# Kernel optimization log

Measured on AMD Instinct MI355X. Metric: run time of the kernel, lower is better.

The kernel has to match this reference:

```python
import math
import jax, jax.numpy as jnp
import numpy as np

B, N_COLS, CHANNELS, NUM_HEADS = 512, 128, 512, 8
D_HEAD = CHANNELS // NUM_HEADS


def setup_inputs() -> dict:
    key = jax.random.key(0)
    ks = jax.random.split(key, 9)
    s = 1.0 / math.sqrt(CHANNELS)
    x = jax.random.normal(ks[0], (B, N_COLS, CHANNELS), dtype=jnp.float32)
    Wq = jax.random.uniform(ks[1], (CHANNELS, CHANNELS), jnp.float32, -s, s)
    bq = jax.random.uniform(ks[2], (CHANNELS,), jnp.float32, -s, s)
    Wk = jax.random.uniform(ks[3], (CHANNELS, CHANNELS), jnp.float32, -s, s)
    bk = jax.random.uniform(ks[4], (CHANNELS,), jnp.float32, -s, s)
    Wv = jax.random.uniform(ks[5], (CHANNELS, CHANNELS), jnp.float32, -s, s)
    bv = jax.random.uniform(ks[6], (CHANNELS,), jnp.float32, -s, s)
    Wo = jax.random.uniform(ks[7], (CHANNELS, CHANNELS), jnp.float32, -s, s)
    bo = jax.random.uniform(ks[8], (CHANNELS,), jnp.float32, -s, s)
    return {"x": x, "Wq": Wq, "bq": bq, "Wk": Wk, "bk": bk,
            "Wv": Wv, "bv": bv, "Wo": Wo, "bo": bo}


def reference(x, Wq, bq, Wk, bk, Wv, bv, Wo, bo):
    b, n, c = x.shape
    h, d = NUM_HEADS, D_HEAD

    def split_heads(t):  # [b, n, c] -> [b, h, n, d]
        return t.reshape(b, n, h, d).transpose(0, 2, 1, 3)

    Q = split_heads(x @ Wq + bq)
    K = split_heads(x @ Wk + bk)
    V = split_heads(x @ Wv + bv)

    # raw scores [b, h, q, k]
    scores = jnp.einsum('bhqd,bhkd->bhqk', Q, K)
    # causal mask over columns; note: mask added BEFORE scaling by sqrt(d)
    causal = jnp.tril(jnp.ones((n, n), dtype=jnp.float32))
    mask = (1.0 - causal) * -100000.0
    attn = jax.nn.softmax((scores + mask) / math.sqrt(d), axis=-1)
    out = jnp.einsum('bhqk,bhkd->bhqd', attn, V)
    out = out.transpose(0, 2, 1, 3).reshape(b, n, c)
    return out @ Wo + bo
```

## Files before the change

### kernel.cpp

```cpp
#include <hip/hip_runtime.h>

typedef _Float16 f16;
typedef _Float16 half8 __attribute__((ext_vector_type(8)));
typedef _Float16 half4 __attribute__((ext_vector_type(4)));
typedef float f32x4 __attribute__((ext_vector_type(4)));

#define B_SZ 512
#define NQ   128
#define CH   512
#define NH   8
#define DH   64
#define MTOK (B_SZ*NQ)
#define KD   512

#define MFMA16(a,b,c) __builtin_amdgcn_mfma_f32_16x16x32_f16((a),(b),(c),0,0,0)

#define GLDS16(g,l) __builtin_amdgcn_global_load_lds( \
    (__attribute__((address_space(1))) void*)(g), \
    (__attribute__((address_space(3))) void*)(l), 16, 0, 0)

__global__ __launch_bounds__(256) void k_cvt(const float* __restrict__ x,
                                             f16* __restrict__ xb) {
  const int n8 = MTOK * KD / 8;
  int i = blockIdx.x * blockDim.x + threadIdx.x;
  const int stride = gridDim.x * blockDim.x;
  for (; i < n8; i += stride) {
    f32x4 a = ((const f32x4*)x)[2 * i];
    f32x4 b = ((const f32x4*)x)[2 * i + 1];
    half8 h;
    h[0] = (f16)a[0]; h[1] = (f16)a[1]; h[2] = (f16)a[2]; h[3] = (f16)a[3];
    h[4] = (f16)b[0]; h[5] = (f16)b[1]; h[6] = (f16)b[2]; h[7] = (f16)b[3];
    ((half8*)xb)[i] = h;
  }
}

__global__ __launch_bounds__(256) void k_wt(const float* __restrict__ Wq,
                                            const float* __restrict__ Wk,
                                            const float* __restrict__ Wv,
                                            const float* __restrict__ Wo,
                                            f16* __restrict__ wt) {
  const int n = blockIdx.x;
  const float* W = (n < 512) ? Wq : (n < 1024) ? Wk : (n < 1536) ? Wv : Wo;
  const int c = n & 511;
  for (int k = threadIdx.x; k < 512; k += blockDim.x)
    wt[n * 512 + k] = (f16)W[k * 512 + c];
}

__global__ __launch_bounds__(256, 2) void k_qkv(
    f16* __restrict__ A, f16* __restrict__ Bw,
    const float* __restrict__ bq, const float* __restrict__ bk,
    const float* __restrict__ bv,
    f16* __restrict__ qb, f16* __restrict__ kb, f16* __restrict__ vb) {
  __shared__ f16 la[128 * 32];
  __shared__ f16 lb[128 * 32];
  const int tid = threadIdx.x;
  const int w = tid >> 6, lane = tid & 63;
  const int ln = lane & 15, g = lane >> 4;
  const int wr = w >> 1, wc = w & 1;
  const int mtile = blockIdx.y, ntile = blockIdx.x;

  const int e0 = w * 512 + lane * 8;
  const int srow = e0 >> 5, scol = e0 & 31;
  f16* gA = A + (mtile * 128 + srow) * KD + scol;
  f16* gB = Bw + (ntile * 128 + srow) * KD + scol;
  f16* lA = la + w * 512;
  f16* lB = lb + w * 512;

  f32x4 acc[4][4] = {};

  for (int kt = 0; kt < 16; ++kt) {
    const int k0 = kt * 32;
    GLDS16(gA + k0, lA);
    GLDS16(gA + 64 * KD + k0, lA + 2048);
    GLDS16(gB + k0, lB);
    GLDS16(gB + 64 * KD + k0, lB + 2048);
    __syncthreads();
    half8 af[4], bf[4];
#pragma unroll
    for (int m = 0; m < 4; ++m)
      af[m] = *(const half8*)(la + (wr * 64 + m * 16 + ln) * 32 + g * 8);
#pragma unroll
    for (int n = 0; n < 4; ++n)
      bf[n] = *(const half8*)(lb + (wc * 64 + n * 16 + ln) * 32 + g * 8);
#pragma unroll
    for (int m = 0; m < 4; ++m)
#pragma unroll
      for (int n = 0; n < 4; ++n)
        acc[m][n] = MFMA16(af[m], bf[n], acc[m][n]);
    __syncthreads();
  }

  const int b = mtile;
  const int colbase = ntile * 128 + wc * 64;
#pragma unroll
  for (int m = 0; m < 4; ++m) {
    const int nn0 = wr * 64 + m * 16 + g * 4;
#pragma unroll
    for (int n = 0; n < 4; ++n) {
      const int col = colbase + n * 16 + ln;
      const int which = col >> 9;
      const int c = col & 511;
      const int h = c >> 6, d = c & 63;
      const float bias = (which == 0) ? bq[c] : (which == 1) ? bk[c] : bv[c];
      if (which < 2) {
        f16* dst = ((which == 0) ? qb : kb) + ((b * NH + h) * NQ + nn0) * DH + d;
#pragma unroll
        for (int r = 0; r < 4; ++r)
          dst[r * DH] = (f16)(acc[m][n][r] + bias);
      } else {
        half4 v4;
#pragma unroll
        for (int r = 0; r < 4; ++r)
          v4[r] = (f16)(acc[m][n][r] + bias);
        *(half4*)(vb + ((b * NH + h) * DH + d) * NQ + nn0) = v4;
      }
    }
  }
}

__global__ __launch_bounds__(256, 2) void k_attn(
    const f16* __restrict__ qbuf, const f16* __restrict__ kbuf,
    const f16* __restrict__ vbuf, f16* __restrict__ ao) {
  __shared__ f16 kl[128 * 72];
  __shared__ f16 vl[64 * 136];
  __shared__ f16 pl[128 * 136];
  const int bh = blockIdx.x;
  const f16* Qp = qbuf + bh * (NQ * DH);
  const f16* Kp = kbuf + bh * (NQ * DH);
  const f16* Vp = vbuf + bh * (DH * NQ);
  const int tid = threadIdx.x;
  const int w = tid >> 6, lane = tid & 63;
  const int ln = lane & 15, g = lane >> 4;

#pragma unroll
  for (int i = 0; i < 4; ++i) {
    const int e = i * 2048 + tid * 8;
    *(half8*)(kl + (e >> 6) * 72 + (e & 63)) = *(const half8*)(Kp + e);
  }
#pragma unroll
  for (int i = 0; i < 4; ++i) {
    const int e = i * 2048 + tid * 8;
    *(half8*)(vl + (e >> 7) * 136 + (e & 127)) = *(const half8*)(Vp + e);
  }
  half8 qf[2][2];
#pragma unroll
  for (int m = 0; m < 2; ++m)
#pragma unroll
    for (int ks = 0; ks < 2; ++ks)
      qf[m][ks] = *(const half8*)(Qp + (w * 32 + m * 16 + ln) * DH + ks * 32 + g * 8);
  __syncthreads();

  f32x4 s[2][8] = {};
#pragma unroll
  for (int ks = 0; ks < 2; ++ks)
#pragma unroll
    for (int n = 0; n < 8; ++n) {
      half8 kf = *(const half8*)(kl + (n * 16 + ln) * 72 + ks * 32 + g * 8);
      s[0][n] = MFMA16(qf[0][ks], kf, s[0][n]);
      s[1][n] = MFMA16(qf[1][ks], kf, s[1][n]);
    }

  float inv[2][4];
#pragma unroll
  for (int m = 0; m < 2; ++m) {
#pragma unroll
    for (int r = 0; r < 4; ++r) {
      const int q = w * 32 + m * 16 + g * 4 + r;
      float z[8];
      float rm = -1e30f;
#pragma unroll
      for (int n = 0; n < 8; ++n) {
        const int col = n * 16 + ln;
        float zz = s[m][n][r] * 0.125f + ((col > q) ? -12500.0f : 0.0f);
        z[n] = zz;
        rm = fmaxf(rm, zz);
      }
      rm = fmaxf(rm, __shfl_xor(rm, 1));
      rm = fmaxf(rm, __shfl_xor(rm, 2));
      rm = fmaxf(rm, __shfl_xor(rm, 4));
      rm = fmaxf(rm, __shfl_xor(rm, 8));
      float rs = 0.f;
#pragma unroll
      for (int n = 0; n < 8; ++n) {
        const float p = __expf(z[n] - rm);
        rs += p;
        pl[q * 136 + n * 16 + ln] = (f16)p;
      }
      rs += __shfl_xor(rs, 1);
      rs += __shfl_xor(rs, 2);
      rs += __shfl_xor(rs, 4);
      rs += __shfl_xor(rs, 8);
      inv[m][r] = 1.0f / rs;
    }
  }

  f32x4 o[2][4] = {};
#pragma unroll
  for (int ks = 0; ks < 4; ++ks) {
    half8 pf0 = *(const half8*)(pl + (w * 32 + ln) * 136 + ks * 32 + g * 8);
    half8 pf1 = *(const half8*)(pl + (w * 32 + 16 + ln) * 136 + ks * 32 + g * 8);
#pragma unroll
    for (int n = 0; n < 4; ++n) {
      half8 vf = *(const half8*)(vl + (n * 16 + ln) * 136 + ks * 32 + g * 8);
      o[0][n] = MFMA16(pf0, vf, o[0][n]);
      o[1][n] = MFMA16(pf1, vf, o[1][n]);
    }
  }

  const int b = bh >> 3, h = bh & 7;
  f16* dst = ao + (b * NQ) * CH + h * DH;
#pragma unroll
  for (int m = 0; m < 2; ++m)
#pragma unroll
    for (int n = 0; n < 4; ++n)
#pragma unroll
      for (int r = 0; r < 4; ++r) {
        const int q = w * 32 + m * 16 + g * 4 + r;
        dst[q * CH + n * 16 + ln] = (f16)(o[m][n][r] * inv[m][r]);
      }
}

__global__ __launch_bounds__(256, 2) void k_out(
    f16* __restrict__ A, f16* __restrict__ Bw,
    const float* __restrict__ bo, float* __restrict__ out) {
  __shared__ f16 la[128 * 32];
  __shared__ f16 lb[128 * 32];
  const int tid = threadIdx.x;
  const int w = tid >> 6, lane = tid & 63;
  const int ln = lane & 15, g = lane >> 4;
  const int wr = w >> 1, wc = w & 1;
  const int mtile = blockIdx.y, ntile = blockIdx.x;

  const int e0 = w * 512 + lane * 8;
  const int srow = e0 >> 5, scol = e0 & 31;
  f16* gA = A + (mtile * 128 + srow) * KD + scol;
  f16* gB = Bw + (ntile * 128 + srow) * KD + scol;
  f16* lA = la + w * 512;
  f16* lB = lb + w * 512;

  f32x4 acc[4][4] = {};

  for (int kt = 0; kt < 16; ++kt) {
    const int k0 = kt * 32;
    GLDS16(gA + k0, lA);
    GLDS16(gA + 64 * KD + k0, lA + 2048);
    GLDS16(gB + k0, lB);
    GLDS16(gB + 64 * KD + k0, lB + 2048);
    __syncthreads();
    half8 af[4], bf[4];
#pragma unroll
    for (int m = 0; m < 4; ++m)
      af[m] = *(const half8*)(la + (wr * 64 + m * 16 + ln) * 32 + g * 8);
#pragma unroll
    for (int n = 0; n < 4; ++n)
      bf[n] = *(const half8*)(lb + (wc * 64 + n * 16 + ln) * 32 + g * 8);
#pragma unroll
    for (int m = 0; m < 4; ++m)
#pragma unroll
      for (int n = 0; n < 4; ++n)
        acc[m][n] = MFMA16(af[m], bf[n], acc[m][n]);
    __syncthreads();
  }

  const int colbase = ntile * 128 + wc * 64;
#pragma unroll
  for (int m = 0; m < 4; ++m) {
    const int tok0 = mtile * 128 + wr * 64 + m * 16 + g * 4;
#pragma unroll
    for (int n = 0; n < 4; ++n) {
      const int col = colbase + n * 16 + ln;
      const float bias = bo[col];
      float* dst = out + tok0 * CH + col;
#pragma unroll
      for (int r = 0; r < 4; ++r)
        dst[r * CH] = acc[m][n][r] + bias;
    }
  }
}

extern "C" void kernel_launch(void* const* d_in, const int* in_sizes, int n_in,
                              void* d_out, int out_size, void* d_ws, size_t ws_size,
                              hipStream_t stream) {
  (void)in_sizes; (void)n_in; (void)out_size; (void)ws_size;
  const float* x  = (const float*)d_in[0];
  const float* Wq = (const float*)d_in[1];
  const float* bq = (const float*)d_in[2];
  const float* Wk = (const float*)d_in[3];
  const float* bk = (const float*)d_in[4];
  const float* Wv = (const float*)d_in[5];
  const float* bv = (const float*)d_in[6];
  const float* Wo = (const float*)d_in[7];
  const float* bo = (const float*)d_in[8];
  float* out = (float*)d_out;

  char* ws = (char*)d_ws;
  const size_t SZ = (size_t)MTOK * KD * sizeof(f16);
  f16* xb = (f16*)(ws);
  f16* qb = (f16*)(ws + SZ);
  f16* kb = (f16*)(ws + 2 * SZ);
  f16* vb = (f16*)(ws + 3 * SZ);
  f16* wt = (f16*)(ws + 4 * SZ);
  f16* ao = xb;

  k_cvt<<<2048, 256, 0, stream>>>(x, xb);
  k_wt<<<2048, 256, 0, stream>>>(Wq, Wk, Wv, Wo, wt);
  k_qkv<<<dim3(12, 512), 256, 0, stream>>>(xb, wt, bq, bk, bv, qb, kb, vb);
  k_attn<<<4096, 256, 0, stream>>>(qb, kb, vb, ao);
  k_out<<<dim3(4, 512), 256, 0, stream>>>(ao, wt + 1536 * KD, bo, out);
}
```

Before: 328.4 us.

## Replace projection GEMMs with double-buffered 256x256 tiled MFMA pipeline

```diff
diff --git a/kernel.cpp b/kernel.cpp
--- a/kernel.cpp
+++ b/kernel.cpp
@@ -46,74 +46,183 @@
     wt[n * 512 + k] = (f16)W[k * 512 + c];
 }
 
-__global__ __launch_bounds__(256, 2) void k_qkv(
-    f16* __restrict__ A, f16* __restrict__ Bw,
+
+template<bool SW, int MB>
+__device__ __forceinline__ void mfma16x(f32x4 (&acc)[8][4], half8 (&af)[4], half8 (&bf)[4]) {
+#pragma unroll
+  for (int i = 0; i < 4; ++i)
+#pragma unroll
+    for (int n = 0; n < 4; ++n) {
+      if (SW) acc[MB + i][n] = MFMA16(bf[n], af[i], acc[MB + i][n]);
+      else    acc[MB + i][n] = MFMA16(af[i], bf[n], acc[MB + i][n]);
+    }
+}
+
+__device__ __forceinline__ void load4(const f16* base, half8 (&fr)[4]) {
+#pragma unroll
+  for (int n = 0; n < 4; ++n) fr[n] = *(const half8*)(base + n * 512);
+}
+
+#define BAR_MFMA_OPEN() __builtin_amdgcn_s_barrier(); \
+  asm volatile("s_waitcnt lgkmcnt(0)" ::: "memory"); \
+  __builtin_amdgcn_sched_barrier(0); \
+  __builtin_amdgcn_s_setprio(1)
+#define MFMA_CLOSE() __builtin_amdgcn_s_setprio(0); __builtin_amdgcn_s_barrier()
+#define MFMA_CLOSE_GATE4() __builtin_amdgcn_s_setprio(0); \
+  asm volatile("s_waitcnt vmcnt(4)" ::: "memory"); \
+  __builtin_amdgcn_s_barrier()
+#define MFMA_CLOSE_GATE0() __builtin_amdgcn_s_setprio(0); \
+  asm volatile("s_waitcnt vmcnt(0)" ::: "memory"); \
+  __builtin_amdgcn_s_barrier()
+
+template<bool SW>
+__device__ __forceinline__ void gemm256_main(
+    const f16* __restrict__ Ag, const f16* __restrict__ Bg,
+    int arow0, f16* lds, f32x4 (&acc)[8][4]) {
+  const int tid = threadIdx.x;
+  const int w = tid >> 6, lane = tid & 63;
+  const int ln = lane & 15, g = lane >> 4;
+  const int wm = w >> 2, wn = w & 3;
+  const int slotx = ((g ^ ((ln >> 1) & 3)) << 3);
+
+  f16* la = lds;
+  f16* lb = lds + 32768;
+
+  const int gsrc = (((tid & 3) ^ ((tid >> 3) & 3)) << 3);
+  int soA[4], soB[4];
+#pragma unroll
+  for (int ks2 = 0; ks2 < 2; ++ks2)
+#pragma unroll
+    for (int r = 0; r < 2; ++r) {
+      soA[ks2 * 2 + r] = (arow0 + r * 128 + (tid >> 2)) * KD + ks2 * 32 + gsrc;
+      soB[ks2 * 2 + r] = (r * 128 + (tid >> 2)) * KD + ks2 * 32 + gsrc;
+    }
+  const int ldst = w * 512;
+
+#define STAGE_A(t, ks2, r) GLDS16((f16*)Ag + soA[(ks2)*2+(r)] + (t)*64, \
+      la + ((t)&1)*16384 + (ks2)*8192 + (r)*4096 + ldst)
+#define STAGE_B(t, ks2, r) GLDS16((f16*)Bg + soB[(ks2)*2+(r)] + (t)*64, \
+      lb + ((t)&1)*16384 + (ks2)*8192 + (r)*4096 + ldst)
+
+  const int raA = (wm * 128 + ln) * 32 + slotx;
+  const int raB = (wn * 64 + ln) * 32 + slotx;
+
+  STAGE_A(0, 0, 0); STAGE_A(0, 0, 1); STAGE_B(0, 0, 0); STAGE_B(0, 0, 1);
+  STAGE_A(0, 1, 0); STAGE_A(0, 1, 1); STAGE_B(0, 1, 0); STAGE_B(0, 1, 1);
+  asm volatile("s_waitcnt vmcnt(0)" ::: "memory");
+  __builtin_amdgcn_s_barrier();
+
+  half8 af[4], bf[4];
+
+#pragma unroll 1
+  for (int t = 0; t < 7; ++t) {
+    const int cur = t & 1;
+    const f16* lac = la + cur * 16384;
+    const f16* lbc = lb + cur * 16384;
+    load4(lbc + raB, bf);
+    load4(lac + raA, af);
+    STAGE_A(t + 1, 0, 0); STAGE_A(t + 1, 0, 1);
+    BAR_MFMA_OPEN(); mfma16x<SW, 0>(acc, af, bf); MFMA_CLOSE();
+    load4(lac + raA + 4 * 512, af);
+    STAGE_B(t + 1, 0, 0); STAGE_B(t + 1, 0, 1);
+    BAR_MFMA_OPEN(); mfma16x<SW, 4>(acc, af, bf); MFMA_CLOSE_GATE4();
+    load4(lbc + 8192 + raB, bf);
+    load4(lac + 8192 + raA, af);
+    STAGE_A(t + 1, 1, 0); STAGE_A(t + 1, 1, 1);
+    BAR_MFMA_OPEN(); mfma16x<SW, 0>(acc, af, bf); MFMA_CLOSE();
+    load4(lac + 8192 + raA + 4 * 512, af);
+    STAGE_B(t + 1, 1, 0); STAGE_B(t + 1, 1, 1);
+    BAR_MFMA_OPEN(); mfma16x<SW, 4>(acc, af, bf); MFMA_CLOSE_GATE4();
+  }
+  {
+    const f16* lac = la + 16384;
+    const f16* lbc = lb + 16384;
+    load4(lbc + raB, bf);
+    load4(lac + raA, af);
+    BAR_MFMA_OPEN(); mfma16x<SW, 0>(acc, af, bf); MFMA_CLOSE();
+    load4(lac + raA + 4 * 512, af);
+    BAR_MFMA_OPEN(); mfma16x<SW, 4>(acc, af, bf); MFMA_CLOSE_GATE0();
+    load4(lbc + 8192 + raB, bf);
+    load4(lac + 8192 + raA, af);
+    BAR_MFMA_OPEN(); mfma16x<SW, 0>(acc, af, bf); MFMA_CLOSE();
+    load4(lac + 8192 + raA + 4 * 512, af);
+    __builtin_amdgcn_s_barrier();
+    asm volatile("s_waitcnt lgkmcnt(0)" ::: "memory");
+    __builtin_amdgcn_sched_barrier(0);
+    mfma16x<SW, 4>(acc, af, bf);
+  }
+#undef STAGE_A
+#undef STAGE_B
+}
+
+__global__ __launch_bounds__(512, 2) void k_qk256(
+    const f16* __restrict__ A, const f16* __restrict__ wt,
     const float* __restrict__ bq, const float* __restrict__ bk,
-    const float* __restrict__ bv,
-    f16* __restrict__ qb, f16* __restrict__ kb, f16* __restrict__ vb) {
-  __shared__ f16 la[128 * 32];
-  __shared__ f16 lb[128 * 32];
-  const int tid = threadIdx.x;
-  const int w = tid >> 6, lane = tid & 63;
-  const int ln = lane & 15, g = lane >> 4;
-  const int wr = w >> 1, wc = w & 1;
-  const int mtile = blockIdx.y, ntile = blockIdx.x;
-
-  const int e0 = w * 512 + lane * 8;
-  const int srow = e0 >> 5, scol = e0 & 31;
-  f16* gA = A + (mtile * 128 + srow) * KD + scol;
-  f16* gB = Bw + (ntile * 128 + srow) * KD + scol;
-  f16* lA = la + w * 512;
-  f16* lB = lb + w * 512;
-
-  f32x4 acc[4][4] = {};
-
-  for (int kt = 0; kt < 16; ++kt) {
-    const int k0 = kt * 32;
-    GLDS16(gA + k0, lA);
-    GLDS16(gA + 64 * KD + k0, lA + 2048);
-    GLDS16(gB + k0, lB);
-    GLDS16(gB + 64 * KD + k0, lB + 2048);
-    __syncthreads();
-    half8 af[4], bf[4];
-#pragma unroll
-    for (int m = 0; m < 4; ++m)
-      af[m] = *(const half8*)(la + (wr * 64 + m * 16 + ln) * 32 + g * 8);
-#pragma unroll
-    for (int n = 0; n < 4; ++n)
-      bf[n] = *(const half8*)(lb + (wc * 64 + n * 16 + ln) * 32 + g * 8);
-#pragma unroll
-    for (int m = 0; m < 4; ++m)
-#pragma unroll
-      for (int n = 0; n < 4; ++n)
-        acc[m][n] = MFMA16(af[m], bf[n], acc[m][n]);
-    __syncthreads();
-  }
-
-  const int b = mtile;
-  const int colbase = ntile * 128 + wc * 64;
-#pragma unroll
-  for (int m = 0; m < 4; ++m) {
-    const int nn0 = wr * 64 + m * 16 + g * 4;
-#pragma unroll
-    for (int n = 0; n < 4; ++n) {
-      const int col = colbase + n * 16 + ln;
-      const int which = col >> 9;
-      const int c = col & 511;
-      const int h = c >> 6, d = c & 63;
-      const float bias = (which == 0) ? bq[c] : (which == 1) ? bk[c] : bv[c];
-      if (which < 2) {
-        f16* dst = ((which == 0) ? qb : kb) + ((b * NH + h) * NQ + nn0) * DH + d;
-#pragma unroll
-        for (int r = 0; r < 4; ++r)
-          dst[r * DH] = (f16)(acc[m][n][r] + bias);
-      } else {
-        half4 v4;
-#pragma unroll
-        for (int r = 0; r < 4; ++r)
-          v4[r] = (f16)(acc[m][n][r] + bias);
-        *(half4*)(vb + ((b * NH + h) * DH + d) * NQ + nn0) = v4;
-      }
+    f16* __restrict__ qb, f16* __restrict__ kb) {
+  __shared__ f16 smem[65536];
+  const int nwg8 = 1024 / 8;
+  const int f = (blockIdx.x & 7) * nwg8 + (blockIdx.x >> 3);
+  const int ntile = f & 3, mtile = f >> 2;
+  const int arow0 = mtile * 256;
+  const f16* Bg = wt + ntile * 256 * KD;
+
+  f32x4 acc[8][4] = {};
+  gemm256_main<true>(A, Bg, arow0, smem, acc);
+
+  const int tid = threadIdx.x;
+  const int w = tid >> 6, lane = tid & 63;
+  const int ln = lane & 15, g = lane >> 4;
+  const int wm = w >> 2, wn = w & 3;
+  const int cslab = (ntile & 1) << 8;
+  const float* bias = (ntile < 2) ? bq : bk;
+  f16* dst = (ntile < 2) ? qb : kb;
+#pragma unroll
+  for (int n = 0; n < 4; ++n) {
+    const int cg = cslab + wn * 64 + n * 16 + g * 4;
+    const f32x4 b4 = *(const f32x4*)(bias + cg);
+    const int h = cg >> 6, d = cg & 63;
+#pragma unroll
+    for (int m = 0; m < 8; ++m) {
+      const int tk = arow0 + wm * 128 + m * 16 + ln;
+      const int b = tk >> 7, tr = tk & 127;
+      half4 o;
+#pragma unroll
+      for (int r = 0; r < 4; ++r) o[r] = (f16)(acc[m][n][r] + b4[r]);
+      *(half4*)(dst + ((b * NH + h) * NQ + tr) * DH + d) = o;
+    }
+  }
+}
+
+__global__ __launch_bounds__(512, 2) void k_v256(
+    const f16* __restrict__ A, const f16* __restrict__ wt,
+    const float* __restrict__ bv, f16* __restrict__ vb) {
+  __shared__ f16 smem[65536];
+  const int nwg8 = 512 / 8;
+  const int f = (blockIdx.x & 7) * nwg8 + (blockIdx.x >> 3);
+  const int ntile = f & 1, mtile = f >> 1;
+  const int arow0 = mtile * 256;
+  const f16* Bg = wt + (1024 + ntile * 256) * KD;
+
+  f32x4 acc[8][4] = {};
+  gemm256_main<false>(A, Bg, arow0, smem, acc);
+
+  const int tid = threadIdx.x;
+  const int w = tid >> 6, lane = tid & 63;
+  const int ln = lane & 15, g = lane >> 4;
+  const int wm = w >> 2, wn = w & 3;
+#pragma unroll
+  for (int n = 0; n < 4; ++n) {
+    const int cg = ntile * 256 + wn * 64 + n * 16 + ln;
+    const float bias = bv[cg];
+    const int h = cg >> 6, d = cg & 63;
+#pragma unroll
+    for (int m = 0; m < 8; ++m) {
+      const int t0 = arow0 + wm * 128 + m * 16 + g * 4;
+      const int b = t0 >> 7, tr = t0 & 127;
+      half4 o;
+#pragma unroll
+      for (int r = 0; r < 4; ++r) o[r] = (f16)(acc[m][n][r] + bias);
+      *(half4*)(vb + ((b * NH + h) * DH + d) * NQ + tr) = o;
     }
   }
 }
@@ -220,60 +329,32 @@
       }
 }
 
-__global__ __launch_bounds__(256, 2) void k_out(
-    f16* __restrict__ A, f16* __restrict__ Bw,
+__global__ __launch_bounds__(512, 2) void k_out256(
+    const f16* __restrict__ A, const f16* __restrict__ wt,
     const float* __restrict__ bo, float* __restrict__ out) {
-  __shared__ f16 la[128 * 32];
-  __shared__ f16 lb[128 * 32];
-  const int tid = threadIdx.x;
-  const int w = tid >> 6, lane = tid & 63;
-  const int ln = lane & 15, g = lane >> 4;
-  const int wr = w >> 1, wc = w & 1;
-  const int mtile = blockIdx.y, ntile = blockIdx.x;
-
-  const int e0 = w * 512 + lane * 8;
-  const int srow = e0 >> 5, scol = e0 & 31;
-  f16* gA = A + (mtile * 128 + srow) * KD + scol;
-  f16* gB = Bw + (ntile * 128 + srow) * KD + scol;
-  f16* lA = la + w * 512;
-  f16* lB = lb + w * 512;
-
-  f32x4 acc[4][4] = {};
-
-  for (int kt = 0; kt < 16; ++kt) {
-    const int k0 = kt * 32;
-    GLDS16(gA + k0, lA);
-    GLDS16(gA + 64 * KD + k0, lA + 2048);
-    GLDS16(gB + k0, lB);
-    GLDS16(gB + 64 * KD + k0, lB + 2048);
-    __syncthreads();
-    half8 af[4], bf[4];
-#pragma unroll
-    for (int m = 0; m < 4; ++m)
-      af[m] = *(const half8*)(la + (wr * 64 + m * 16 + ln) * 32 + g * 8);
-#pragma unroll
-    for (int n = 0; n < 4; ++n)
-      bf[n] = *(const half8*)(lb + (wc * 64 + n * 16 + ln) * 32 + g * 8);
-#pragma unroll
-    for (int m = 0; m < 4; ++m)
-#pragma unroll
-      for (int n = 0; n < 4; ++n)
-        acc[m][n] = MFMA16(af[m], bf[n], acc[m][n]);
-    __syncthreads();
-  }
-
-  const int colbase = ntile * 128 + wc * 64;
-#pragma unroll
-  for (int m = 0; m < 4; ++m) {
-    const int tok0 = mtile * 128 + wr * 64 + m * 16 + g * 4;
-#pragma unroll
-    for (int n = 0; n < 4; ++n) {
-      const int col = colbase + n * 16 + ln;
-      const float bias = bo[col];
-      float* dst = out + tok0 * CH + col;
-#pragma unroll
-      for (int r = 0; r < 4; ++r)
-        dst[r * CH] = acc[m][n][r] + bias;
+  __shared__ f16 smem[65536];
+  const int nwg8 = 512 / 8;
+  const int f = (blockIdx.x & 7) * nwg8 + (blockIdx.x >> 3);
+  const int ntile = f & 1, mtile = f >> 1;
+  const int arow0 = mtile * 256;
+  const f16* Bg = wt + (1536 + ntile * 256) * KD;
+
+  f32x4 acc[8][4] = {};
+  gemm256_main<true>(A, Bg, arow0, smem, acc);
+
+  const int tid = threadIdx.x;
+  const int w = tid >> 6, lane = tid & 63;
+  const int ln = lane & 15, g = lane >> 4;
+  const int wm = w >> 2, wn = w & 3;
+#pragma unroll
+  for (int n = 0; n < 4; ++n) {
+    const int cg = ntile * 256 + wn * 64 + n * 16 + g * 4;
+    const f32x4 b4 = *(const f32x4*)(bo + cg);
+#pragma unroll
+    for (int m = 0; m < 8; ++m) {
+      const int tk = arow0 + wm * 128 + m * 16 + ln;
+      f32x4 o = acc[m][n] + b4;
+      *(f32x4*)(out + tk * CH + cg) = o;
     }
   }
 }
@@ -304,7 +385,8 @@
 
   k_cvt<<<2048, 256, 0, stream>>>(x, xb);
   k_wt<<<2048, 256, 0, stream>>>(Wq, Wk, Wv, Wo, wt);
-  k_qkv<<<dim3(12, 512), 256, 0, stream>>>(xb, wt, bq, bk, bv, qb, kb, vb);
+  k_qk256<<<1024, 512, 0, stream>>>(xb, wt, bq, bk, qb, kb);
+  k_v256<<<512, 512, 0, stream>>>(xb, wt, bv, vb);
   k_attn<<<4096, 256, 0, stream>>>(qb, kb, vb, ao);
-  k_out<<<dim3(4, 512), 256, 0, stream>>>(ao, wt + 1536 * KD, bo, out);
-}
+  k_out256<<<512, 512, 0, stream>>>(ao, wt, bo, out);
+}
```

Measured after the change: 330.0 us. About the same (+0.5%).

## Swizzle GEMM LDS layout, remap block indices for XCD locality, raise occupancy

Applied to the files above, without the earlier changes.

```diff
diff --git a/kernel.cpp b/kernel.cpp
--- a/kernel.cpp
+++ b/kernel.cpp
@@ -46,8 +46,8 @@
     wt[n * 512 + k] = (f16)W[k * 512 + c];
 }
 
-__global__ __launch_bounds__(256, 2) void k_qkv(
-    f16* __restrict__ A, f16* __restrict__ Bw,
+__global__ __launch_bounds__(256, 4) void k_qkv(
+    const f16* __restrict__ A, const f16* __restrict__ Bw,
     const float* __restrict__ bq, const float* __restrict__ bk,
     const float* __restrict__ bv,
     f16* __restrict__ qb, f16* __restrict__ kb, f16* __restrict__ vb) {
@@ -57,14 +57,18 @@
   const int w = tid >> 6, lane = tid & 63;
   const int ln = lane & 15, g = lane >> 4;
   const int wr = w >> 1, wc = w & 1;
-  const int mtile = blockIdx.y, ntile = blockIdx.x;
-
-  const int e0 = w * 512 + lane * 8;
-  const int srow = e0 >> 5, scol = e0 & 31;
-  f16* gA = A + (mtile * 128 + srow) * KD + scol;
-  f16* gB = Bw + (ntile * 128 + srow) * KD + scol;
+  const int s = blockIdx.x >> 3;
+  const int ml = s / 12;
+  const int ntile = s - ml * 12;
+  const int mtile = (blockIdx.x & 7) * 64 + ml;
+
+  const int srow = w * 16 + (lane >> 2);
+  const int scol = ((lane & 3) ^ ((lane >> 3) & 3)) * 8;
+  const f16* gA = A + (mtile * 128 + srow) * KD + scol;
+  const f16* gB = Bw + (ntile * 128 + srow) * KD + scol;
   f16* lA = la + w * 512;
   f16* lB = lb + w * 512;
+  const int slotx = (g ^ ((ln >> 1) & 3)) * 8;
 
   f32x4 acc[4][4] = {};
 
@@ -78,10 +82,10 @@
     half8 af[4], bf[4];
 #pragma unroll
     for (int m = 0; m < 4; ++m)
-      af[m] = *(const half8*)(la + (wr * 64 + m * 16 + ln) * 32 + g * 8);
+      af[m] = *(const half8*)(la + (wr * 64 + m * 16 + ln) * 32 + slotx);
 #pragma unroll
     for (int n = 0; n < 4; ++n)
-      bf[n] = *(const half8*)(lb + (wc * 64 + n * 16 + ln) * 32 + g * 8);
+      bf[n] = *(const half8*)(lb + (wc * 64 + n * 16 + ln) * 32 + slotx);
 #pragma unroll
     for (int m = 0; m < 4; ++m)
 #pragma unroll
@@ -220,8 +224,8 @@
       }
 }
 
-__global__ __launch_bounds__(256, 2) void k_out(
-    f16* __restrict__ A, f16* __restrict__ Bw,
+__global__ __launch_bounds__(256, 4) void k_out(
+    const f16* __restrict__ A, const f16* __restrict__ Bw,
     const float* __restrict__ bo, float* __restrict__ out) {
   __shared__ f16 la[128 * 32];
   __shared__ f16 lb[128 * 32];
@@ -229,14 +233,18 @@
   const int w = tid >> 6, lane = tid & 63;
   const int ln = lane & 15, g = lane >> 4;
   const int wr = w >> 1, wc = w & 1;
-  const int mtile = blockIdx.y, ntile = blockIdx.x;
-
-  const int e0 = w * 512 + lane * 8;
-  const int srow = e0 >> 5, scol = e0 & 31;
-  f16* gA = A + (mtile * 128 + srow) * KD + scol;
-  f16* gB = Bw + (ntile * 128 + srow) * KD + scol;
+  const int s = blockIdx.x >> 3;
+  const int ml = s >> 2;
+  const int ntile = s & 3;
+  const int mtile = (blockIdx.x & 7) * 64 + ml;
+
+  const int srow = w * 16 + (lane >> 2);
+  const int scol = ((lane & 3) ^ ((lane >> 3) & 3)) * 8;
+  const f16* gA = A + (mtile * 128 + srow) * KD + scol;
+  const f16* gB = Bw + (ntile * 128 + srow) * KD + scol;
   f16* lA = la + w * 512;
   f16* lB = lb + w * 512;
+  const int slotx = (g ^ ((ln >> 1) & 3)) * 8;
 
   f32x4 acc[4][4] = {};
 
@@ -250,10 +258,10 @@
     half8 af[4], bf[4];
 #pragma unroll
     for (int m = 0; m < 4; ++m)
-      af[m] = *(const half8*)(la + (wr * 64 + m * 16 + ln) * 32 + g * 8);
+      af[m] = *(const half8*)(la + (wr * 64 + m * 16 + ln) * 32 + slotx);
 #pragma unroll
     for (int n = 0; n < 4; ++n)
-      bf[n] = *(const half8*)(lb + (wc * 64 + n * 16 + ln) * 32 + g * 8);
+      bf[n] = *(const half8*)(lb + (wc * 64 + n * 16 + ln) * 32 + slotx);
 #pragma unroll
     for (int m = 0; m < 4; ++m)
 #pragma unroll
@@ -304,7 +312,7 @@
 
   k_cvt<<<2048, 256, 0, stream>>>(x, xb);
   k_wt<<<2048, 256, 0, stream>>>(Wq, Wk, Wv, Wo, wt);
-  k_qkv<<<dim3(12, 512), 256, 0, stream>>>(xb, wt, bq, bk, bv, qb, kb, vb);
+  k_qkv<<<6144, 256, 0, stream>>>(xb, wt, bq, bk, bv, qb, kb, vb);
   k_attn<<<4096, 256, 0, stream>>>(qb, kb, vb, ao);
-  k_out<<<dim3(4, 512), 256, 0, stream>>>(ao, wt + 1536 * KD, bo, out);
-}
+  k_out<<<2048, 256, 0, stream>>>(ao, wt + 1536 * KD, bo, out);
+}
```

Result: faster. 309.5 us (-5.8%).
